# Optimization experiments

Measured on AMD Instinct MI355X. Metric: run time of the kernel, lower is better.

Reference implementation:

```python
import jax, jax.numpy as jnp
import numpy as np

B, NC, NF, D = 4, 256, 768, 768
TOK_RATIO = 0.5
LN_EPS = 1e-5


def _linear(x, w, b):
    # w: [D_in, D_out]
    return x @ w + b


def _leaky(x):
    return jax.nn.leaky_relu(x, negative_slope=0.01)


def setup_inputs() -> dict:
    key = jax.random.key(0)
    ks = jax.random.split(key, 12)
    s = 1.0 / np.sqrt(D)
    inp = {
        "cls_tokens": jax.random.normal(ks[0], (B, NC, D), dtype=jnp.float32),
        "feats": jax.random.normal(ks[1], (B, NF, D), dtype=jnp.float32),
        "W_head_w": jax.random.uniform(ks[2], (D, D), minval=-s, maxval=s),
        "W_head_b": jax.random.uniform(ks[3], (D,), minval=-s, maxval=s),
        "W_tail_w": jax.random.uniform(ks[4], (D, D), minval=-s, maxval=s),
        "W_tail_b": jax.random.uniform(ks[5], (D,), minval=-s, maxval=s),
        "lin1_w": jax.random.uniform(ks[6], (D, D), minval=-s, maxval=s),
        "lin1_b": jax.random.uniform(ks[7], (D,), minval=-s, maxval=s),
        "lin2_w": jax.random.uniform(ks[8], (D, D), minval=-s, maxval=s),
        "lin2_b": jax.random.uniform(ks[9], (D,), minval=-s, maxval=s),
        "ln_w": jnp.ones((D,), dtype=jnp.float32),
        "ln_b": jnp.zeros((D,), dtype=jnp.float32),
    }
    return inp


def reference(cls_tokens, feats, W_head_w, W_head_b, W_tail_w, W_tail_b,
              lin1_w, lin1_b, lin2_w, lin2_b, ln_w, ln_b):
    topk = int(TOK_RATIO * NC)
    scale = D ** (-0.5)

    # feats is detached in the original (clone().detach())
    x = jnp.concatenate([cls_tokens, jax.lax.stop_gradient(feats)], axis=1)  # [B, Nt, D]

    e_h = _linear(cls_tokens, W_head_w, W_head_b)  # [B, Nc, D]
    e_t = _linear(x, W_tail_w, W_tail_b)           # [B, Nt, D]

    attn_logit = jnp.einsum('bnd,bmd->bnm', e_h * scale, e_t)  # [B, Nc, Nt]
    topk_weight, topk_index = jax.lax.top_k(attn_logit, topk)  # [B, Nc, k]

    # Gather neighbor embeddings: Nb_h[b, n, j] = e_t[b, topk_index[b, n, j]]
    Nb_h = jax.vmap(lambda et, idx: et[idx])(e_t, topk_index)  # [B, Nc, k, D]

    topk_prob = jax.nn.softmax(topk_weight, axis=2)            # [B, Nc, k]
    p = topk_prob[..., None]
    eh_r = p * Nb_h + (1.0 - p) * e_h[:, :, None, :]           # [B, Nc, k, D]

    gate = jnp.tanh(e_h[:, :, None, :] + eh_r)
    ka_weight = jnp.einsum('bnkd,bnkd->bnk', Nb_h, gate)
    ka_prob = jax.nn.softmax(ka_weight, axis=2)
    e_Nh = jnp.einsum('bnk,bnkd->bnd', ka_prob, Nb_h)          # [B, Nc, D]

    # bi-interaction aggregation
    sum_emb = _leaky(_linear((e_h + e_Nh) * 0.1 + cls_tokens, lin1_w, lin1_b))
    bi_emb = _leaky(_linear(e_h * e_Nh * 0.1 + cls_tokens, lin2_w, lin2_b))
    embedding = sum_emb + bi_emb

    # LayerNorm (dropout is a no-op: p=0 and output overwritten in original)
    mu = jnp.mean(embedding, axis=-1, keepdims=True)
    var = jnp.var(embedding, axis=-1, keepdims=True)
    h = (embedding - mu) * jax.lax.rsqrt(var + LN_EPS) * ln_w + ln_b
    return h
```

## Files before the change

### kernel.cpp

```cpp
#include <hip/hip_runtime.h>
#include <hip/hip_bf16.h>
#include <math.h>

#define DDIM 768
#define NCLS 256
#define NFEAT 768
#define NTOK 1024
#define NBATCH 4
#define KSEL 128

typedef float f32x4 __attribute__((ext_vector_type(4)));
typedef short s16x8 __attribute__((ext_vector_type(8)));

__device__ __forceinline__ float wsum(float v) {
#pragma unroll
  for (int o = 32; o; o >>= 1) v += __shfl_down(v, o, 64);
  return v;
}
__device__ __forceinline__ float wmaxr(float v) {
#pragma unroll
  for (int o = 32; o; o >>= 1) v = fmaxf(v, __shfl_down(v, o, 64));
  return v;
}
__device__ __forceinline__ short f2bf(float f) {
  union { __hip_bfloat16 h; short s; } u;
  u.h = __float2bfloat16(f);
  return u.s;
}
__device__ __forceinline__ float bf2f(short s) {
  union { unsigned u; float f; } c;
  c.u = ((unsigned)(unsigned short)s) << 16;
  return c.f;
}
__device__ __forceinline__ void cvt8(float4 x, float4 y, s16x8& h, s16x8& l) {
  float v[8] = {x.x, x.y, x.z, x.w, y.x, y.y, y.z, y.w};
#pragma unroll
  for (int i = 0; i < 8; ++i) {
    short hh = f2bf(v[i]);
    h[i] = hh;
    l[i] = f2bf(v[i] - bf2f(hh));
  }
}
__device__ __forceinline__ int swz(int row, int chunk) {
  return (row << 5) + (((chunk ^ (row >> 1)) & 3) << 3);
}

__global__ __launch_bounds__(256) void xprep(const float* __restrict__ cls,
                                             const float* __restrict__ feats,
                                             short* __restrict__ Xh,
                                             short* __restrict__ Xl) {
  const size_t base = ((size_t)blockIdx.x * 256 + threadIdx.x) * 8;
  const int row = (int)(base / DDIM);
  const int col = (int)(base % DDIM);
  const int b = row >> 10, rr = row & 1023;
  const float* src = (rr < NCLS)
                         ? cls + ((size_t)b * NCLS + rr) * DDIM + col
                         : feats + ((size_t)b * NFEAT + (rr - NCLS)) * DDIM + col;
  float4 a0 = *(const float4*)(src);
  float4 a1 = *(const float4*)(src + 4);
  s16x8 h, l;
  cvt8(a0, a1, h, l);
  *(s16x8*)(Xh + base) = h;
  *(s16x8*)(Xl + base) = l;
}

__global__ __launch_bounds__(256) void prep_weights(
    const float* __restrict__ w0, const float* __restrict__ w1,
    const float* __restrict__ w2, const float* __restrict__ w3,
    short* __restrict__ h0, short* __restrict__ h1, short* __restrict__ h2,
    short* __restrict__ h3, short* __restrict__ l0, short* __restrict__ l1) {
  __shared__ float tile[32][33];
  const int z = blockIdx.z;
  const float* s = z == 0 ? w0 : z == 1 ? w1 : z == 2 ? w2 : w3;
  short* dh = z == 0 ? h0 : z == 1 ? h1 : z == 2 ? h2 : h3;
  short* dl = z == 0 ? l0 : z == 1 ? l1 : nullptr;
  const int tx = threadIdx.x & 31, ty0 = threadIdx.x >> 5;
  const int r0 = blockIdx.y * 32, c0 = blockIdx.x * 32;
#pragma unroll
  for (int i = 0; i < 4; ++i) {
    int ty = ty0 + i * 8;
    tile[ty][tx] = s[(size_t)(r0 + ty) * DDIM + c0 + tx];
  }
  __syncthreads();
#pragma unroll
  for (int i = 0; i < 4; ++i) {
    int ty = ty0 + i * 8;
    float v = tile[tx][ty];
    short hh = f2bf(v);
    dh[(size_t)(c0 + ty) * DDIM + r0 + tx] = hh;
    if (dl) dl[(size_t)(c0 + ty) * DDIM + r0 + tx] = f2bf(v - bf2f(hh));
  }
}

__global__ __launch_bounds__(256) void gemm_front(
    const short* __restrict__ Xh, const short* __restrict__ Xl,
    const short* __restrict__ WhT_h, const short* __restrict__ WhT_l,
    const float* __restrict__ Whb, const short* __restrict__ WtT_h,
    const short* __restrict__ WtT_l, const float* __restrict__ Wtb,
    short* __restrict__ eh_hi, short* __restrict__ eh_lo,
    short* __restrict__ et_hi, short* __restrict__ et_lo) {
  __shared__ short Ah[128 * 32], Al[128 * 32];
  __shared__ short Bh[64 * 32], Bl[64 * 32];
  const int bid = blockIdx.x;
  const int xcd = bid & 7, idx = bid >> 3;
  const int ytile = xcd * 5 + idx / 12;
  const int xtile = idx % 12;
  const int t = threadIdx.x;
  const int row0 = ytile * 128, col0 = xtile * 64;
  const bool head = row0 < 1024;

  const int ar = t >> 1, ac = (t & 1) * 2;
  const int aw0 = swz(ar, ac), aw1 = swz(ar, ac + 1);
  size_t xrow;
  {
    int gr = row0 + ar;
    xrow = head ? (size_t)(((gr >> 8) << 10) + (gr & 255)) : (size_t)(gr - 1024);
  }
  const short* aph = Xh + xrow * DDIM + ac * 8;
  const short* apl = Xl + xrow * DDIM + ac * 8;
  const int br = t >> 2, bc = t & 3;
  const int bw0 = swz(br, bc);
  const short* bph = (head ? WhT_h : WtT_h) + (size_t)(col0 + br) * DDIM + bc * 8;
  const short* bpl = (head ? WhT_l : WtT_l) + (size_t)(col0 + br) * DDIM + bc * 8;
  const float* biasu = head ? Whb : Wtb;

  const int lane = t & 63, wave = t >> 6;
  const int wr = wave >> 1, wc = wave & 1;
  const int fr = lane & 15, fq = lane >> 4;

  f32x4 acc[4][2] = {};
  s16x8 rah0 = *(const s16x8*)(aph);
  s16x8 rah1 = *(const s16x8*)(aph + 8);
  s16x8 ral0 = *(const s16x8*)(apl);
  s16x8 ral1 = *(const s16x8*)(apl + 8);
  s16x8 rbh = *(const s16x8*)(bph);
  s16x8 rbl = *(const s16x8*)(bpl);

  for (int kt = 0; kt < 24; ++kt) {
    __syncthreads();
    *(s16x8*)&Ah[aw0] = rah0;
    *(s16x8*)&Ah[aw1] = rah1;
    *(s16x8*)&Al[aw0] = ral0;
    *(s16x8*)&Al[aw1] = ral1;
    *(s16x8*)&Bh[bw0] = rbh;
    *(s16x8*)&Bl[bw0] = rbl;
    __syncthreads();
    const int kn = (kt < 23 ? kt + 1 : 23) * 32;
    rah0 = *(const s16x8*)(aph + kn);
    rah1 = *(const s16x8*)(aph + kn + 8);
    ral0 = *(const s16x8*)(apl + kn);
    ral1 = *(const s16x8*)(apl + kn + 8);
    rbh = *(const s16x8*)(bph + kn);
    rbl = *(const s16x8*)(bpl + kn);

    s16x8 afh[4], afl[4];
#pragma unroll
    for (int m = 0; m < 4; ++m) {
      int ao = swz(wr * 64 + m * 16 + fr, fq);
      afh[m] = *(const s16x8*)&Ah[ao];
      afl[m] = *(const s16x8*)&Al[ao];
    }
#pragma unroll
    for (int n = 0; n < 2; ++n) {
      int bo = swz(wc * 32 + n * 16 + fr, fq);
      s16x8 bfh = *(const s16x8*)&Bh[bo];
      s16x8 bfl = *(const s16x8*)&Bl[bo];
#pragma unroll
      for (int m = 0; m < 4; ++m) {
        acc[m][n] =
            __builtin_amdgcn_mfma_f32_16x16x32_bf16(afh[m], bfh, acc[m][n], 0, 0, 0);
        acc[m][n] =
            __builtin_amdgcn_mfma_f32_16x16x32_bf16(afh[m], bfl, acc[m][n], 0, 0, 0);
        acc[m][n] =
            __builtin_amdgcn_mfma_f32_16x16x32_bf16(afl[m], bfh, acc[m][n], 0, 0, 0);
      }
    }
  }

  short* Ch = head ? eh_hi : et_hi;
  short* Cl = head ? eh_lo : et_lo;
  const int rbase = head ? row0 : row0 - 1024;
#pragma unroll
  for (int m = 0; m < 4; ++m) {
#pragma unroll
    for (int n = 0; n < 2; ++n) {
#pragma unroll
      for (int r = 0; r < 4; ++r) {
        int rg = rbase + wr * 64 + m * 16 + fq * 4 + r;
        int cg = col0 + wc * 32 + n * 16 + fr;
        float v = acc[m][n][r] + biasu[cg];
        size_t o = (size_t)rg * DDIM + cg;
        short hh = f2bf(v);
        Ch[o] = hh;
        Cl[o] = f2bf(v - bf2f(hh));
      }
    }
  }
}

__global__ __launch_bounds__(256) void gemm_logits(
    const short* __restrict__ eh_hi, const short* __restrict__ eh_lo,
    const short* __restrict__ et_hi, const short* __restrict__ et_lo,
    float* __restrict__ logits, float scale) {
  __shared__ short Ah[32 * 32], Al[32 * 32];
  __shared__ short Bh[64 * 32], Bl[64 * 32];
  const int bid = blockIdx.x;
  const int xcd = bid & 7, idx = bid >> 3;
  const int batch = xcd >> 1;
  const int sub = ((xcd & 1) << 6) | idx;
  const int xtile = sub & 15, ytile = sub >> 4;
  const int row0 = ytile * 32, col0 = xtile * 64;
  const int t = threadIdx.x;

  const int ahalf = t >> 7, ac2 = t & 127;
  const int asr = ac2 >> 2, acc_ = ac2 & 3;
  const short* aptr = (ahalf ? eh_lo : eh_hi) +
                      ((size_t)batch * NCLS + row0 + asr) * DDIM + acc_ * 8;
  const int aso = swz(asr, acc_);
  const int bsr = t >> 2, bcc = t & 3;
  const short* bph = et_hi + ((size_t)batch * NTOK + col0 + bsr) * DDIM + bcc * 8;
  const short* bpl = et_lo + ((size_t)batch * NTOK + col0 + bsr) * DDIM + bcc * 8;
  const int bso = swz(bsr, bcc);

  const int lane = t & 63, wave = t >> 6;
  const int wr = wave >> 1, wc = wave & 1;
  const int fr = lane & 15, fq = lane >> 4;

  f32x4 acc[2] = {};
  s16x8 rA = *(const s16x8*)(aptr);
  s16x8 rbh = *(const s16x8*)(bph);
  s16x8 rbl = *(const s16x8*)(bpl);

  for (int kt = 0; kt < 24; ++kt) {
    __syncthreads();
    *(s16x8*)&(ahalf ? Al : Ah)[aso] = rA;
    *(s16x8*)&Bh[bso] = rbh;
    *(s16x8*)&Bl[bso] = rbl;
    __syncthreads();
    const int kn = (kt < 23 ? kt + 1 : 23) * 32;
    rA = *(const s16x8*)(aptr + kn);
    rbh = *(const s16x8*)(bph + kn);
    rbl = *(const s16x8*)(bpl + kn);
    int ao = swz(wr * 16 + fr, fq);
    s16x8 afh = *(const s16x8*)&Ah[ao];
    s16x8 afl = *(const s16x8*)&Al[ao];
#pragma unroll
    for (int n = 0; n < 2; ++n) {
      int bo = swz(wc * 32 + n * 16 + fr, fq);
      s16x8 bfh = *(const s16x8*)&Bh[bo];
      s16x8 bfl = *(const s16x8*)&Bl[bo];
      acc[n] = __builtin_amdgcn_mfma_f32_16x16x32_bf16(afh, bfh, acc[n], 0, 0, 0);
      acc[n] = __builtin_amdgcn_mfma_f32_16x16x32_bf16(afh, bfl, acc[n], 0, 0, 0);
      acc[n] = __builtin_amdgcn_mfma_f32_16x16x32_bf16(afl, bfh, acc[n], 0, 0, 0);
    }
  }

  float* Cb = logits + (size_t)batch * NCLS * NTOK;
#pragma unroll
  for (int n = 0; n < 2; ++n)
#pragma unroll
    for (int r = 0; r < 4; ++r) {
      int rg = row0 + wr * 16 + fq * 4 + r;
      int cg = col0 + wc * 32 + n * 16 + fr;
      Cb[(size_t)rg * NTOK + cg] = scale * acc[n][r];
    }
}

__global__ __launch_bounds__(256) void gemm_lin(
    const short* __restrict__ inbf, const short* __restrict__ L1T,
    const short* __restrict__ L2T, const float* __restrict__ b1,
    const float* __restrict__ b2, float* __restrict__ C) {
  __shared__ short Ah[64 * 32], Bh[64 * 32];
  const int bid = blockIdx.x;
  const int xcd = bid & 7, idx = bid >> 3;
  const int ytile = xcd * 4 + idx / 12, xtile = idx % 12;
  const int t = threadIdx.x;
  const int row0 = ytile * 64, col0 = xtile * 64;
  const bool second = row0 >= 1024;
  const int sr = t >> 2, sc = t & 3;
  const short* aptr = inbf + (size_t)(row0 + sr) * DDIM + sc * 8;
  const short* bptr = (second ? L2T : L1T) + (size_t)(col0 + sr) * DDIM + sc * 8;
  const float* biasu = second ? b2 : b1;
  const int lane = t & 63, wave = t >> 6;
  const int wr = wave >> 1, wc = wave & 1;
  const int fr = lane & 15, fq = lane >> 4;
  const int so = swz(sr, sc);

  f32x4 acc[2][2] = {};
  s16x8 rA = *(const s16x8*)(aptr);
  s16x8 rB = *(const s16x8*)(bptr);
  for (int kt = 0; kt < 24; ++kt) {
    __syncthreads();
    *(s16x8*)&Ah[so] = rA;
    *(s16x8*)&Bh[so] = rB;
    __syncthreads();
    const int kn = (kt < 23 ? kt + 1 : 23) * 32;
    rA = *(const s16x8*)(aptr + kn);
    rB = *(const s16x8*)(bptr + kn);
#pragma unroll
    for (int n = 0; n < 2; ++n) {
      int bo = swz(wc * 32 + n * 16 + fr, fq);
      s16x8 bfh = *(const s16x8*)&Bh[bo];
#pragma unroll
      for (int m = 0; m < 2; ++m) {
        int ao = swz(wr * 32 + m * 16 + fr, fq);
        s16x8 afh = *(const s16x8*)&Ah[ao];
        acc[m][n] =
            __builtin_amdgcn_mfma_f32_16x16x32_bf16(afh, bfh, acc[m][n], 0, 0, 0);
      }
    }
  }
#pragma unroll
  for (int m = 0; m < 2; ++m)
#pragma unroll
    for (int n = 0; n < 2; ++n)
#pragma unroll
      for (int r = 0; r < 4; ++r) {
        int rg = row0 + wr * 32 + m * 16 + fq * 4 + r;
        int cg = col0 + wc * 32 + n * 16 + fr;
        float v = acc[m][n][r] + biasu[cg];
        v = v > 0.f ? v : 0.01f * v;
        C[(size_t)rg * DDIM + cg] = v;
      }
}

__global__ __launch_bounds__(256) void topk_select(
    const float* __restrict__ logits, float* __restrict__ tw,
    int* __restrict__ ti) {
  const int row = blockIdx.x;
  const int t = threadIdx.x;
  const int lane = t & 63, wave = t >> 6;
  __shared__ int hist[256];
  __shared__ int sh_bin, sh_rem;
  __shared__ int cnt;
  __shared__ int wsumT[4];

  float4 v4 = *(const float4*)(logits + (size_t)row * NTOK + 4 * t);
  float val[4] = {v4.x, v4.y, v4.z, v4.w};
  unsigned key[4];
#pragma unroll
  for (int i = 0; i < 4; ++i) {
    unsigned u = __float_as_uint(val[i]);
    key[i] = (u & 0x80000000u) ? ~u : (u | 0x80000000u);
  }

  unsigned pref = 0, mask = 0;
  int rem = KSEL;
#pragma unroll
  for (int shift = 24; shift >= 0; shift -= 8) {
    hist[t] = 0;
    __syncthreads();
#pragma unroll
    for (int i = 0; i < 4; ++i)
      if ((key[i] & mask) == pref)
        atomicAdd(&hist[(key[i] >> shift) & 255], 1);
    __syncthreads();
    if (wave == 0) {
      int h0 = hist[4 * lane], h1 = hist[4 * lane + 1];
      int h2 = hist[4 * lane + 2], h3 = hist[4 * lane + 3];
      int s = h0 + h1 + h2 + h3;
#pragma unroll
      for (int o = 1; o < 64; o <<= 1) {
        int v = __shfl_down(s, o, 64);
        if (lane + o < 64) s += v;
      }
      int abv = __shfl_down(s, 1, 64);
      if (lane == 63) abv = 0;
      int c3 = abv + h3, c2 = c3 + h2, c1 = c2 + h1, c0 = c1 + h0;
      int bin = -1, nab = 0;
      if (c3 >= rem && abv < rem) { bin = 4 * lane + 3; nab = abv; }
      else if (c2 >= rem && c3 < rem) { bin = 4 * lane + 2; nab = c3; }
      else if (c1 >= rem && c2 < rem) { bin = 4 * lane + 1; nab = c2; }
      else if (c0 >= rem && c1 < rem) { bin = 4 * lane + 0; nab = c1; }
      if (bin >= 0) { sh_bin = bin; sh_rem = rem - nab; }
    }
    __syncthreads();
    pref |= ((unsigned)sh_bin) << shift;
    mask |= 0xFFu << shift;
    rem = sh_rem;
  }

  const unsigned T = pref;
  const int above = KSEL - rem;

  if (t == 0) cnt = 0;
  int tc = 0;
#pragma unroll
  for (int i = 0; i < 4; ++i) tc += (key[i] == T);
  int inc = tc;
#pragma unroll
  for (int o = 1; o < 64; o <<= 1) {
    int v = __shfl_up(inc, o, 64);
    if (lane >= o) inc += v;
  }
  if (lane == 63) wsumT[wave] = inc;
  __syncthreads();
  int wbase = 0;
#pragma unroll
  for (int w = 0; w < 4; ++w)
    if (w < wave) wbase += wsumT[w];
  int excl = wbase + inc - tc;

  float* twr = tw + (size_t)row * KSEL;
  int* tir = ti + (size_t)row * KSEL;
#pragma unroll
  for (int i = 0; i < 4; ++i) {
    if (key[i] > T) {
      int slot = atomicAdd(&cnt, 1);
      twr[slot] = val[i];
      tir[slot] = 4 * t + i;
    } else if (key[i] == T) {
      int r = excl++;
      if (r < rem) {
        twr[above + r] = val[i];
        tir[above + r] = 4 * t + i;
      }
    }
  }
}

__global__ __launch_bounds__(256) void agg1(const short* __restrict__ eh_hi,
                                            const short* __restrict__ et_hi,
                                            const float* __restrict__ tw,
                                            const int* __restrict__ ti,
                                            float* __restrict__ kaw_raw) {
  const int bid = blockIdx.x;
  const int xcd = bid & 7, slot = bid >> 3;
  const int batch = xcd >> 1;
  const int u = ((xcd & 1) << 8) | slot;
  const int row = batch * 256 + (u >> 1);
  const int half = u & 1;
  const int t = threadIdx.x, lane = t & 63, wave = t >> 6;
  __shared__ float p[KSEL];
  __shared__ int idxs[KSEL];
  __shared__ float red[2];

  if (t < KSEL) {
    p[t] = tw[(size_t)row * KSEL + t];
    idxs[t] = ti[(size_t)row * KSEL + t];
  }
  __syncthreads();
  if (wave == 0) {
    float m = wmaxr(fmaxf(p[lane], p[lane + 64]));
    if (!lane) red[0] = m;
  }
  __syncthreads();
  if (t < KSEL) p[t] = __expf(p[t] - red[0]);
  __syncthreads();
  if (wave == 0) {
    float s = wsum(p[lane] + p[lane + 64]);
    if (!lane) red[1] = s;
  }
  __syncthreads();
  if (t < KSEL) p[t] *= (1.f / red[1]);
  __syncthreads();

  float ehr[12];
  {
    const short* ehrow = eh_hi + (size_t)row * DDIM;
#pragma unroll
    for (int c = 0; c < 3; ++c) {
      short4 v = *(const short4*)(ehrow + 4 * lane + 256 * c);
      ehr[4 * c + 0] = bf2f(v.x);
      ehr[4 * c + 1] = bf2f(v.y);
      ehr[4 * c + 2] = bf2f(v.z);
      ehr[4 * c + 3] = bf2f(v.w);
    }
  }
  const short* etb = et_hi + (size_t)batch * NTOK * DDIM;

  for (int i = 0; i < 16; ++i) {
    int j = half * 64 + wave * 16 + i;
    float pj = p[j];
    float a = 4.f - 2.f * pj, b2 = 2.f * pj;
    const short* nb = etb + (size_t)idxs[j] * DDIM;
    float partial = 0.f;
#pragma unroll
    for (int c = 0; c < 3; ++c) {
      short4 nv = *(const short4*)(nb + 4 * lane + 256 * c);
      float nq[4] = {bf2f(nv.x), bf2f(nv.y), bf2f(nv.z), bf2f(nv.w)};
#pragma unroll
      for (int q = 0; q < 4; ++q) {
        float y2 = fmaf(a, ehr[4 * c + q], b2 * nq[q]);
        float ex = __expf(y2);
        float g = fmaf(-2.f, __builtin_amdgcn_rcpf(1.f + ex), 1.f);
        partial = fmaf(nq[q], g, partial);
      }
    }
    partial = wsum(partial);
    if (!lane) kaw_raw[(size_t)row * KSEL + j] = partial;
  }
}

__global__ __launch_bounds__(192) void agg2(
    const short* __restrict__ eh_hi, const short* __restrict__ et_hi,
    const float* __restrict__ cls, const float* __restrict__ kaw_raw,
    const int* __restrict__ ti, short* __restrict__ inbf) {
  const int bid = blockIdx.x;
  const int xcd = bid & 7, slot = bid >> 3;
  const int batch = xcd >> 1;
  const int row = batch * 256 + (xcd & 1) * 128 + slot;
  const int t = threadIdx.x, lane = t & 63, wave = t >> 6;
  __shared__ float kp[KSEL];
  __shared__ int idxs[KSEL];
  __shared__ float red[2];

  if (t < KSEL) {
    kp[t] = kaw_raw[(size_t)row * KSEL + t];
    idxs[t] = ti[(size_t)row * KSEL + t];
  }
  __syncthreads();
  if (wave == 0) {
    float m = wmaxr(fmaxf(kp[lane], kp[lane + 64]));
    if (!lane) red[0] = m;
  }
  __syncthreads();
  if (t < KSEL) kp[t] = __expf(kp[t] - red[0]);
  __syncthreads();
  if (wave == 0) {
    float s = wsum(kp[lane] + kp[lane + 64]);
    if (!lane) red[1] = s;
  }
  __syncthreads();
  if (t < KSEL) kp[t] *= (1.f / red[1]);
  __syncthreads();

  const size_t o = (size_t)row * DDIM + 4 * t;
  short4 ehs = *(const short4*)(eh_hi + o);
  float4 eh4 = {bf2f(ehs.x), bf2f(ehs.y), bf2f(ehs.z), bf2f(ehs.w)};
  float4 cl4 = *(const float4*)(cls + o);
  const short* etb = et_hi + (size_t)batch * NTOK * DDIM;

  float ax = 0.f, ay = 0.f, az = 0.f, aw = 0.f;
#pragma unroll 8
  for (int j = 0; j < KSEL; ++j) {
    float pr = kp[j];
    short4 nb = *(const short4*)(etb + (size_t)idxs[j] * DDIM + 4 * t);
    ax = fmaf(pr, bf2f(nb.x), ax);
    ay = fmaf(pr, bf2f(nb.y), ay);
    az = fmaf(pr, bf2f(nb.z), az);
    aw = fmaf(pr, bf2f(nb.w), aw);
  }

  short4 sv, bv;
  sv.x = f2bf((eh4.x + ax) * 0.1f + cl4.x);
  sv.y = f2bf((eh4.y + ay) * 0.1f + cl4.y);
  sv.z = f2bf((eh4.z + az) * 0.1f + cl4.z);
  sv.w = f2bf((eh4.w + aw) * 0.1f + cl4.w);
  bv.x = f2bf((eh4.x * ax) * 0.1f + cl4.x);
  bv.y = f2bf((eh4.y * ay) * 0.1f + cl4.y);
  bv.z = f2bf((eh4.z * az) * 0.1f + cl4.z);
  bv.w = f2bf((eh4.w * aw) * 0.1f + cl4.w);
  *(short4*)&inbf[o] = sv;
  *(short4*)&inbf[(size_t)(NBATCH * NCLS) * DDIM + o] = bv;
}

__global__ __launch_bounds__(256) void ln_kernel(const float* __restrict__ embA,
                                                 const float* __restrict__ embB,
                                                 const float* __restrict__ lw,
                                                 const float* __restrict__ lb,
                                                 float* __restrict__ out) {
  const int row = blockIdx.x;
  const int t = threadIdx.x;
  const int lane = t & 63, wave = t >> 6;
  __shared__ float red[4];
  __shared__ float bs[2];
  float e[3];
#pragma unroll
  for (int c = 0; c < 3; ++c) {
    size_t o = (size_t)row * DDIM + t + 256 * c;
    e[c] = embA[o] + embB[o];
  }
  float s = e[0] + e[1] + e[2];
  s = wsum(s);
  if (lane == 0) red[wave] = s;
  __syncthreads();
  if (t == 0) bs[0] = (red[0] + red[1] + red[2] + red[3]) * (1.f / DDIM);
  __syncthreads();
  float mu = bs[0];
  float q = 0.f;
#pragma unroll
  for (int c = 0; c < 3; ++c) {
    float d = e[c] - mu;
    q = fmaf(d, d, q);
  }
  q = wsum(q);
  if (lane == 0) red[wave] = q;
  __syncthreads();
  if (t == 0) bs[1] = (red[0] + red[1] + red[2] + red[3]) * (1.f / DDIM);
  __syncthreads();
  float rstd = rsqrtf(bs[1] + 1e-5f);
#pragma unroll
  for (int c = 0; c < 3; ++c) {
    int d = t + 256 * c;
    out[(size_t)row * DDIM + d] = (e[c] - mu) * rstd * lw[d] + lb[d];
  }
}

extern "C" void kernel_launch(void* const* d_in, const int* in_sizes, int n_in,
                              void* d_out, int out_size, void* d_ws,
                              size_t ws_size, hipStream_t stream) {
  const float* cls = (const float*)d_in[0];
  const float* feats = (const float*)d_in[1];
  const float* Whw = (const float*)d_in[2];
  const float* Whb = (const float*)d_in[3];
  const float* Wtw = (const float*)d_in[4];
  const float* Wtb = (const float*)d_in[5];
  const float* l1w = (const float*)d_in[6];
  const float* l1b = (const float*)d_in[7];
  const float* l2w = (const float*)d_in[8];
  const float* l2b = (const float*)d_in[9];
  const float* lnw = (const float*)d_in[10];
  const float* lnb = (const float*)d_in[11];
  float* out = (float*)d_out;

  float* ws = (float*)d_ws;
  float* linC = ws;
  short* eh_hi = (short*)(ws + 3932160);
  short* eh_lo = eh_hi + 786432;
  short* et_hi = (short*)(ws + 4718592);
  short* et_lo = et_hi + 3145728;
  short* WhT_h = (short*)(ws + 7864320);
  short* WhT_l = WhT_h + 589824;
  short* WtT_h = WhT_h + 2 * 589824;
  short* WtT_l = WhT_h + 3 * 589824;
  short* L1T = (short*)(ws + 9043968);
  short* L2T = L1T + 589824;
  float* logits = ws + 7864320;
  short* Xh = (short*)(ws + 9633792);
  short* Xl = Xh + 3145728;
  float* tw = ws + 9633792;
  int* ti = (int*)(ws + 9764864);
  float* kaw = ws + 9895936;
  short* inbf = (short*)(ws + 10027008);
  (void)ws_size;
  (void)in_sizes;
  (void)n_in;
  (void)out_size;

  const float scale = 0.036084391824351615f;
  dim3 blk(256);

  xprep<<<dim3(1536), blk, 0, stream>>>(cls, feats, Xh, Xl);
  prep_weights<<<dim3(24, 24, 4), blk, 0, stream>>>(
      Whw, Wtw, l1w, l2w, WhT_h, WtT_h, L1T, L2T, WhT_l, WtT_l);
  gemm_front<<<dim3(480), blk, 0, stream>>>(
      Xh, Xl, WhT_h, WhT_l, Whb, WtT_h, WtT_l, Wtb, eh_hi, eh_lo, et_hi,
      et_lo);
  gemm_logits<<<dim3(512), blk, 0, stream>>>(eh_hi, eh_lo, et_hi, et_lo,
                                             logits, scale);
  topk_select<<<dim3(NBATCH * NCLS), blk, 0, stream>>>(logits, tw, ti);
  agg1<<<dim3(2048), blk, 0, stream>>>(eh_hi, et_hi, tw, ti, kaw);
  agg2<<<dim3(1024), dim3(192), 0, stream>>>(eh_hi, et_hi, cls, kaw, ti, inbf);
  gemm_lin<<<dim3(384), blk, 0, stream>>>(inbf, L1T, L2T, l1b, l2b, linC);
  ln_kernel<<<dim3(NBATCH * NCLS), blk, 0, stream>>>(
      linC, linC + (size_t)(NBATCH * NCLS) * DDIM, lnw, lnb, out);
}
```

Before: 125.7 us.

## Merge prep kernels, fuse lin1/lin2 sum in gemm_lin, widen agg1 loads

Combines the input-conversion and weight-transpose kernels into one launch, saving a launch gap. gemm_lin now computes both the lin1 and lin2 products for the same 32-row tile and writes their summed activations, so the [2048x768] intermediate and the extra read in LayerNorm go away. In exchange the per-block A tile shrinks and the B traffic doubles per block. The aggregation kernel also changes its element-to-lane mapping so each row is read with one wider vector load plus a short4 load.

```diff
diff --git a/kernel.cpp b/kernel.cpp
--- a/kernel.cpp
+++ b/kernel.cpp
@@ -45,50 +45,52 @@
   return (row << 5) + (((chunk ^ (row >> 1)) & 3) << 3);
 }
 
-__global__ __launch_bounds__(256) void xprep(const float* __restrict__ cls,
-                                             const float* __restrict__ feats,
-                                             short* __restrict__ Xh,
-                                             short* __restrict__ Xl) {
-  const size_t base = ((size_t)blockIdx.x * 256 + threadIdx.x) * 8;
-  const int row = (int)(base / DDIM);
-  const int col = (int)(base % DDIM);
-  const int b = row >> 10, rr = row & 1023;
-  const float* src = (rr < NCLS)
-                         ? cls + ((size_t)b * NCLS + rr) * DDIM + col
-                         : feats + ((size_t)b * NFEAT + (rr - NCLS)) * DDIM + col;
-  float4 a0 = *(const float4*)(src);
-  float4 a1 = *(const float4*)(src + 4);
-  s16x8 h, l;
-  cvt8(a0, a1, h, l);
-  *(s16x8*)(Xh + base) = h;
-  *(s16x8*)(Xl + base) = l;
-}
-
-__global__ __launch_bounds__(256) void prep_weights(
+__global__ __launch_bounds__(256) void prep_all(
+    const float* __restrict__ cls, const float* __restrict__ feats,
     const float* __restrict__ w0, const float* __restrict__ w1,
     const float* __restrict__ w2, const float* __restrict__ w3,
     short* __restrict__ h0, short* __restrict__ h1, short* __restrict__ h2,
-    short* __restrict__ h3, short* __restrict__ l0, short* __restrict__ l1) {
+    short* __restrict__ h3, short* __restrict__ l0, short* __restrict__ l1,
+    short* __restrict__ Xh, short* __restrict__ Xl) {
   __shared__ float tile[32][33];
-  const int z = blockIdx.z;
-  const float* s = z == 0 ? w0 : z == 1 ? w1 : z == 2 ? w2 : w3;
-  short* dh = z == 0 ? h0 : z == 1 ? h1 : z == 2 ? h2 : h3;
-  short* dl = z == 0 ? l0 : z == 1 ? l1 : nullptr;
-  const int tx = threadIdx.x & 31, ty0 = threadIdx.x >> 5;
-  const int r0 = blockIdx.y * 32, c0 = blockIdx.x * 32;
-#pragma unroll
-  for (int i = 0; i < 4; ++i) {
-    int ty = ty0 + i * 8;
-    tile[ty][tx] = s[(size_t)(r0 + ty) * DDIM + c0 + tx];
-  }
-  __syncthreads();
-#pragma unroll
-  for (int i = 0; i < 4; ++i) {
-    int ty = ty0 + i * 8;
-    float v = tile[tx][ty];
-    short hh = f2bf(v);
-    dh[(size_t)(c0 + ty) * DDIM + r0 + tx] = hh;
-    if (dl) dl[(size_t)(c0 + ty) * DDIM + r0 + tx] = f2bf(v - bf2f(hh));
+  const int bid = blockIdx.x;
+  const int t = threadIdx.x;
+  if (bid < 2304) {
+    const int z = bid / 576, rem = bid % 576;
+    const int by = rem / 24, bx = rem % 24;
+    const float* s = z == 0 ? w0 : z == 1 ? w1 : z == 2 ? w2 : w3;
+    short* dh = z == 0 ? h0 : z == 1 ? h1 : z == 2 ? h2 : h3;
+    short* dl = z == 0 ? l0 : z == 1 ? l1 : nullptr;
+    const int tx = t & 31, ty0 = t >> 5;
+    const int r0 = by * 32, c0 = bx * 32;
+#pragma unroll
+    for (int i = 0; i < 4; ++i) {
+      int ty = ty0 + i * 8;
+      tile[ty][tx] = s[(size_t)(r0 + ty) * DDIM + c0 + tx];
+    }
+    __syncthreads();
+#pragma unroll
+    for (int i = 0; i < 4; ++i) {
+      int ty = ty0 + i * 8;
+      float v = tile[tx][ty];
+      short hh = f2bf(v);
+      dh[(size_t)(c0 + ty) * DDIM + r0 + tx] = hh;
+      if (dl) dl[(size_t)(c0 + ty) * DDIM + r0 + tx] = f2bf(v - bf2f(hh));
+    }
+  } else {
+    const size_t base = ((size_t)(bid - 2304) * 256 + t) * 8;
+    const int row = (int)(base / DDIM);
+    const int col = (int)(base % DDIM);
+    const int b = row >> 10, rr = row & 1023;
+    const float* src =
+        (rr < NCLS) ? cls + ((size_t)b * NCLS + rr) * DDIM + col
+                    : feats + ((size_t)b * NFEAT + (rr - NCLS)) * DDIM + col;
+    float4 a0 = *(const float4*)(src);
+    float4 a1 = *(const float4*)(src + 4);
+    s16x8 h, l;
+    cvt8(a0, a1, h, l);
+    *(s16x8*)(Xh + base) = h;
+    *(s16x8*)(Xl + base) = l;
   }
 }
 
@@ -269,59 +271,67 @@
 __global__ __launch_bounds__(256) void gemm_lin(
     const short* __restrict__ inbf, const short* __restrict__ L1T,
     const short* __restrict__ L2T, const float* __restrict__ b1,
-    const float* __restrict__ b2, float* __restrict__ C) {
-  __shared__ short Ah[64 * 32], Bh[64 * 32];
+    const float* __restrict__ b2, float* __restrict__ emb) {
+  __shared__ short A1[32 * 32], A2[32 * 32];
+  __shared__ short B1[64 * 32], B2[64 * 32];
   const int bid = blockIdx.x;
   const int xcd = bid & 7, idx = bid >> 3;
   const int ytile = xcd * 4 + idx / 12, xtile = idx % 12;
   const int t = threadIdx.x;
-  const int row0 = ytile * 64, col0 = xtile * 64;
-  const bool second = row0 >= 1024;
-  const int sr = t >> 2, sc = t & 3;
-  const short* aptr = inbf + (size_t)(row0 + sr) * DDIM + sc * 8;
-  const short* bptr = (second ? L2T : L1T) + (size_t)(col0 + sr) * DDIM + sc * 8;
-  const float* biasu = second ? b2 : b1;
+  const int row0 = ytile * 32, col0 = xtile * 64;
+
+  const int ahalf = t >> 7, at = t & 127;
+  const int asr = at >> 2, asc = at & 3;
+  const short* aptr = inbf + (ahalf ? (size_t)1024 * DDIM : 0) +
+                      (size_t)(row0 + asr) * DDIM + asc * 8;
+  const int aso = swz(asr, asc);
+  const int bsr = t >> 2, bsc = t & 3;
+  const short* b1p = L1T + (size_t)(col0 + bsr) * DDIM + bsc * 8;
+  const short* b2p = L2T + (size_t)(col0 + bsr) * DDIM + bsc * 8;
+  const int bso = swz(bsr, bsc);
+
   const int lane = t & 63, wave = t >> 6;
   const int wr = wave >> 1, wc = wave & 1;
   const int fr = lane & 15, fq = lane >> 4;
-  const int so = swz(sr, sc);
-
-  f32x4 acc[2][2] = {};
+
+  f32x4 acc1[2] = {}, acc2[2] = {};
   s16x8 rA = *(const s16x8*)(aptr);
-  s16x8 rB = *(const s16x8*)(bptr);
+  s16x8 rB1 = *(const s16x8*)(b1p);
+  s16x8 rB2 = *(const s16x8*)(b2p);
   for (int kt = 0; kt < 24; ++kt) {
     __syncthreads();
-    *(s16x8*)&Ah[so] = rA;
-    *(s16x8*)&Bh[so] = rB;
+    *(s16x8*)&(ahalf ? A2 : A1)[aso] = rA;
+    *(s16x8*)&B1[bso] = rB1;
+    *(s16x8*)&B2[bso] = rB2;
     __syncthreads();
     const int kn = (kt < 23 ? kt + 1 : 23) * 32;
     rA = *(const s16x8*)(aptr + kn);
-    rB = *(const s16x8*)(bptr + kn);
+    rB1 = *(const s16x8*)(b1p + kn);
+    rB2 = *(const s16x8*)(b2p + kn);
+    int ao = swz(wr * 16 + fr, fq);
+    s16x8 a1f = *(const s16x8*)&A1[ao];
+    s16x8 a2f = *(const s16x8*)&A2[ao];
 #pragma unroll
     for (int n = 0; n < 2; ++n) {
       int bo = swz(wc * 32 + n * 16 + fr, fq);
-      s16x8 bfh = *(const s16x8*)&Bh[bo];
-#pragma unroll
-      for (int m = 0; m < 2; ++m) {
-        int ao = swz(wr * 32 + m * 16 + fr, fq);
-        s16x8 afh = *(const s16x8*)&Ah[ao];
-        acc[m][n] =
-            __builtin_amdgcn_mfma_f32_16x16x32_bf16(afh, bfh, acc[m][n], 0, 0, 0);
-      }
-    }
-  }
-#pragma unroll
-  for (int m = 0; m < 2; ++m)
-#pragma unroll
-    for (int n = 0; n < 2; ++n)
-#pragma unroll
-      for (int r = 0; r < 4; ++r) {
-        int rg = row0 + wr * 32 + m * 16 + fq * 4 + r;
-        int cg = col0 + wc * 32 + n * 16 + fr;
-        float v = acc[m][n][r] + biasu[cg];
-        v = v > 0.f ? v : 0.01f * v;
-        C[(size_t)rg * DDIM + cg] = v;
-      }
+      s16x8 b1f = *(const s16x8*)&B1[bo];
+      s16x8 b2f = *(const s16x8*)&B2[bo];
+      acc1[n] = __builtin_amdgcn_mfma_f32_16x16x32_bf16(a1f, b1f, acc1[n], 0, 0, 0);
+      acc2[n] = __builtin_amdgcn_mfma_f32_16x16x32_bf16(a2f, b2f, acc2[n], 0, 0, 0);
+    }
+  }
+#pragma unroll
+  for (int n = 0; n < 2; ++n)
+#pragma unroll
+    for (int r = 0; r < 4; ++r) {
+      int rg = row0 + wr * 16 + fq * 4 + r;
+      int cg = col0 + wc * 32 + n * 16 + fr;
+      float v1 = acc1[n][r] + b1[cg];
+      v1 = v1 > 0.f ? v1 : 0.01f * v1;
+      float v2 = acc2[n][r] + b2[cg];
+      v2 = v2 > 0.f ? v2 : 0.01f * v2;
+      emb[(size_t)rg * DDIM + cg] = v1 + v2;
+    }
 }
 
 __global__ __launch_bounds__(256) void topk_select(
@@ -458,14 +468,14 @@
   float ehr[12];
   {
     const short* ehrow = eh_hi + (size_t)row * DDIM;
-#pragma unroll
-    for (int c = 0; c < 3; ++c) {
-      short4 v = *(const short4*)(ehrow + 4 * lane + 256 * c);
-      ehr[4 * c + 0] = bf2f(v.x);
-      ehr[4 * c + 1] = bf2f(v.y);
-      ehr[4 * c + 2] = bf2f(v.z);
-      ehr[4 * c + 3] = bf2f(v.w);
-    }
+    s16x8 e8 = *(const s16x8*)(ehrow + 8 * lane);
+    short4 e4 = *(const short4*)(ehrow + 512 + 4 * lane);
+#pragma unroll
+    for (int i = 0; i < 8; ++i) ehr[i] = bf2f(e8[i]);
+    ehr[8] = bf2f(e4.x);
+    ehr[9] = bf2f(e4.y);
+    ehr[10] = bf2f(e4.z);
+    ehr[11] = bf2f(e4.w);
   }
   const short* etb = et_hi + (size_t)batch * NTOK * DDIM;
 
@@ -474,18 +484,22 @@
     float pj = p[j];
     float a = 4.f - 2.f * pj, b2 = 2.f * pj;
     const short* nb = etb + (size_t)idxs[j] * DDIM;
+    s16x8 n8 = *(const s16x8*)(nb + 8 * lane);
+    short4 n4 = *(const short4*)(nb + 512 + 4 * lane);
+    float nq[12];
+#pragma unroll
+    for (int q = 0; q < 8; ++q) nq[q] = bf2f(n8[q]);
+    nq[8] = bf2f(n4.x);
+    nq[9] = bf2f(n4.y);
+    nq[10] = bf2f(n4.z);
+    nq[11] = bf2f(n4.w);
     float partial = 0.f;
 #pragma unroll
-    for (int c = 0; c < 3; ++c) {
-      short4 nv = *(const short4*)(nb + 4 * lane + 256 * c);
-      float nq[4] = {bf2f(nv.x), bf2f(nv.y), bf2f(nv.z), bf2f(nv.w)};
-#pragma unroll
-      for (int q = 0; q < 4; ++q) {
-        float y2 = fmaf(a, ehr[4 * c + q], b2 * nq[q]);
-        float ex = __expf(y2);
-        float g = fmaf(-2.f, __builtin_amdgcn_rcpf(1.f + ex), 1.f);
-        partial = fmaf(nq[q], g, partial);
-      }
+    for (int q = 0; q < 12; ++q) {
+      float y2 = fmaf(a, ehr[q], b2 * nq[q]);
+      float ex = __expf(y2);
+      float g = fmaf(-2.f, __builtin_amdgcn_rcpf(1.f + ex), 1.f);
+      partial = fmaf(nq[q], g, partial);
     }
     partial = wsum(partial);
     if (!lane) kaw_raw[(size_t)row * KSEL + j] = partial;
@@ -555,8 +569,7 @@
   *(short4*)&inbf[(size_t)(NBATCH * NCLS) * DDIM + o] = bv;
 }
 
-__global__ __launch_bounds__(256) void ln_kernel(const float* __restrict__ embA,
-                                                 const float* __restrict__ embB,
+__global__ __launch_bounds__(256) void ln_kernel(const float* __restrict__ emb,
                                                  const float* __restrict__ lw,
                                                  const float* __restrict__ lb,
                                                  float* __restrict__ out) {
@@ -567,10 +580,7 @@
   __shared__ float bs[2];
   float e[3];
 #pragma unroll
-  for (int c = 0; c < 3; ++c) {
-    size_t o = (size_t)row * DDIM + t + 256 * c;
-    e[c] = embA[o] + embB[o];
-  }
+  for (int c = 0; c < 3; ++c) e[c] = emb[(size_t)row * DDIM + t + 256 * c];
   float s = e[0] + e[1] + e[2];
   s = wsum(s);
   if (lane == 0) red[wave] = s;
@@ -615,7 +625,7 @@
   float* out = (float*)d_out;
 
   float* ws = (float*)d_ws;
-  float* linC = ws;
+  float* emb = ws;
   short* eh_hi = (short*)(ws + 3932160);
   short* eh_lo = eh_hi + 786432;
   short* et_hi = (short*)(ws + 4718592);
@@ -641,9 +651,9 @@
   const float scale = 0.036084391824351615f;
   dim3 blk(256);
 
-  xprep<<<dim3(1536), blk, 0, stream>>>(cls, feats, Xh, Xl);
-  prep_weights<<<dim3(24, 24, 4), blk, 0, stream>>>(
-      Whw, Wtw, l1w, l2w, WhT_h, WtT_h, L1T, L2T, WhT_l, WtT_l);
+  prep_all<<<dim3(3840), blk, 0, stream>>>(cls, feats, Whw, Wtw, l1w, l2w,
+                                           WhT_h, WtT_h, L1T, L2T, WhT_l,
+                                           WtT_l, Xh, Xl);
   gemm_front<<<dim3(480), blk, 0, stream>>>(
       Xh, Xl, WhT_h, WhT_l, Whb, WtT_h, WtT_l, Wtb, eh_hi, eh_lo, et_hi,
       et_lo);
@@ -652,7 +662,6 @@
   topk_select<<<dim3(NBATCH * NCLS), blk, 0, stream>>>(logits, tw, ti);
   agg1<<<dim3(2048), blk, 0, stream>>>(eh_hi, et_hi, tw, ti, kaw);
   agg2<<<dim3(1024), dim3(192), 0, stream>>>(eh_hi, et_hi, cls, kaw, ti, inbf);
-  gemm_lin<<<dim3(384), blk, 0, stream>>>(inbf, L1T, L2T, l1b, l2b, linC);
-  ln_kernel<<<dim3(NBATCH * NCLS), blk, 0, stream>>>(
-      linC, linC + (size_t)(NBATCH * NCLS) * DDIM, lnw, lnb, out);
-}
+  gemm_lin<<<dim3(384), blk, 0, stream>>>(inbf, L1T, L2T, l1b, l2b, emb);
+  ln_kernel<<<dim3(NBATCH * NCLS), blk, 0, stream>>>(emb, lnw, lnb, out);
+}
```

Result: no change. 124.2 us (-1.2%).
